# Performance work log

Hardware: AMD Instinct MI355X
Metric: run time of the kernel (lower is better)

## Reference

```python
import jax, jax.numpy as jnp
import numpy as np

K = 3  # kernel size along the folded height sub-dimension

def setup_inputs() -> dict:
    key = jax.random.key(0)
    k1, k2 = jax.random.split(key)
    x = jax.random.normal(k1, (1, 48, 56, 56), dtype=jnp.float32)
    W = jax.random.normal(k2, (192, 48, 3), dtype=jnp.float32)
    return {"x": x, "W": W}

def reference(x, W):
    # x: (1,48,56,56) -> (1,48,8,7,56): split H=56 into (8,7)
    t = x.reshape(1, 48, 8, 7, 56)
    # unfold((3,1), padding=(1,0)) acting on the size-7 axis:
    # pad by 1 on each side, then gather K=3 shifted views.
    tp = jnp.pad(t, ((0, 0), (0, 0), (0, 0), (1, 1), (0, 0)))  # (1,48,8,9,56)
    # patches[l,j,n,k,o,m] = tp[l,j,n,o+k,m], o in [0,7), k in [0,3)
    patches = jnp.stack([tp[:, :, :, k:k + 7, :] for k in range(K)], axis=3)  # (1,48,8,3,7,56)
    # einsum 'ljnkom, ijk -> linom' with W (192,48,3)
    out = jnp.einsum('ljnkom,ijk->linom', patches, W)  # (1,192,8,7,56)
    return out.reshape(1, 192, 56, 56)
```

## Files before the change

kernel.cpp:

```cpp
#include <hip/hip_runtime.h>


#define CH_IN 48
#define CH_OUT 192
#define HW 56
#define SP 3136
#define NB 8
#define OB 7
#define M4 14
#define COLS (NB * M4)
#define NCOL (CH_OUT * COLS)
#define SEGS 4
#define JSEG (CH_IN / SEGS)

__device__ __forceinline__ void fma4(float4& a, float s, const float4& b) {
    a.x += s * b.x; a.y += s * b.y; a.z += s * b.z; a.w += s * b.w;
}
__device__ __forceinline__ void add4(float4& a, const float4& b) {
    a.x += b.x; a.y += b.y; a.z += b.z; a.w += b.w;
}

__global__ __launch_bounds__(256) void conv_split_kernel(const float* __restrict__ x,
                                                         const float* __restrict__ W,
                                                         float* __restrict__ out) {
    __shared__ float4 lds[SEGS][OB][64];

    const int c   = threadIdx.x & 63;
    const int seg = threadIdx.x >> 6;
    const int col = blockIdx.x * 64 + c;

    const int i   = col / COLS;
    const int rem = col % COLS;
    const int n   = rem / M4;
    const int m4  = rem % M4;

    const float* xcol = x + seg * (JSEG * SP) + n * (OB * HW) + m4 * 4;
    const float* wrow = W + i * (CH_IN * 3) + seg * (JSEG * 3);

    float4 acc[OB];
#pragma unroll
    for (int o = 0; o < OB; ++o) acc[o] = make_float4(0.f, 0.f, 0.f, 0.f);

#pragma unroll 4
    for (int j = 0; j < JSEG; ++j) {
        const float w0 = wrow[j * 3 + 0];
        const float w1 = wrow[j * 3 + 1];
        const float w2 = wrow[j * 3 + 2];

        const float* xj = xcol + j * SP;
        float4 xv[OB];
#pragma unroll
        for (int o = 0; o < OB; ++o)
            xv[o] = *reinterpret_cast<const float4*>(xj + o * HW);

#pragma unroll
        for (int o = 0; o < OB; ++o) {
            if (o > 0)      fma4(acc[o], w0, xv[o - 1]);
            fma4(acc[o], w1, xv[o]);
            if (o < OB - 1) fma4(acc[o], w2, xv[o + 1]);
        }
    }

#pragma unroll
    for (int o = 0; o < OB; ++o) lds[seg][o][c] = acc[o];
    __syncthreads();

    for (int t = threadIdx.x; t < OB * 64; t += 256) {
        const int o  = t >> 6;
        const int cc = t & 63;
        float4 s = lds[0][o][cc];
        add4(s, lds[1][o][cc]);
        add4(s, lds[2][o][cc]);
        add4(s, lds[3][o][cc]);

        const int col2 = blockIdx.x * 64 + cc;
        const int i2   = col2 / COLS;
        const int rem2 = col2 % COLS;
        const int n2   = rem2 / M4;
        const int m42  = rem2 % M4;
        *reinterpret_cast<float4*>(out + i2 * SP + n2 * (OB * HW) + o * HW + m42 * 4) = s;
    }
}

extern "C" void kernel_launch(void* const* d_in, const int* in_sizes, int n_in,
                              void* d_out, int out_size, void* d_ws, size_t ws_size,
                              hipStream_t stream) {
    const float* x = (const float*)d_in[0];
    const float* W = (const float*)d_in[1];
    float* out = (float*)d_out;

    const int grid = NCOL / 64;
    conv_split_kernel<<<grid, 256, 0, stream>>>(x, W, out);
}
```

Measured before the change: 62.23 us.

## Split input channels into eight segments with smaller 16-column blocks

Raises the reduction split over input channels from 4 to 8 segments and shrinks each block to 16 output columns with 128 threads, giving 1344 blocks instead of 336. The j loop (now 6 iterations) is fully unrolled. The aim is more parallelism and occupancy across the GPU's compute units. In exchange each block does more LDS reduction work relative to compute, and global loads become narrower because each wavefront covers only 16 columns.

```diff
diff --git a/kernel.cpp b/kernel.cpp
--- a/kernel.cpp
+++ b/kernel.cpp
@@ -5,13 +5,13 @@
 #define CH_OUT 192
 #define HW 56
 #define SP 3136
-#define NB 8
 #define OB 7
 #define M4 14
-#define COLS (NB * M4)
+#define COLS 112
 #define NCOL (CH_OUT * COLS)
-#define SEGS 4
+#define SEGS 8
 #define JSEG (CH_IN / SEGS)
+#define BCOL 16
 
 __device__ __forceinline__ void fma4(float4& a, float s, const float4& b) {
     a.x += s * b.x; a.y += s * b.y; a.z += s * b.z; a.w += s * b.w;
@@ -20,14 +20,14 @@
     a.x += b.x; a.y += b.y; a.z += b.z; a.w += b.w;
 }
 
-__global__ __launch_bounds__(256) void conv_split_kernel(const float* __restrict__ x,
-                                                         const float* __restrict__ W,
-                                                         float* __restrict__ out) {
-    __shared__ float4 lds[SEGS][OB][64];
+__global__ __launch_bounds__(128) void conv_split8_kernel(const float* __restrict__ x,
+                                                          const float* __restrict__ W,
+                                                          float* __restrict__ out) {
+    __shared__ float4 lds[SEGS][OB][BCOL];
 
-    const int c   = threadIdx.x & 63;
-    const int seg = threadIdx.x >> 6;
-    const int col = blockIdx.x * 64 + c;
+    const int c   = threadIdx.x & (BCOL - 1);
+    const int seg = threadIdx.x / BCOL;
+    const int col = blockIdx.x * BCOL + c;
 
     const int i   = col / COLS;
     const int rem = col % COLS;
@@ -41,7 +41,7 @@
 #pragma unroll
     for (int o = 0; o < OB; ++o) acc[o] = make_float4(0.f, 0.f, 0.f, 0.f);
 
-#pragma unroll 4
+#pragma unroll
     for (int j = 0; j < JSEG; ++j) {
         const float w0 = wrow[j * 3 + 0];
         const float w1 = wrow[j * 3 + 1];
@@ -65,15 +65,15 @@
     for (int o = 0; o < OB; ++o) lds[seg][o][c] = acc[o];
     __syncthreads();
 
-    for (int t = threadIdx.x; t < OB * 64; t += 256) {
-        const int o  = t >> 6;
-        const int cc = t & 63;
+    const int t = threadIdx.x;
+    if (t < OB * BCOL) {
+        const int o  = t / BCOL;
+        const int cc = t & (BCOL - 1);
         float4 s = lds[0][o][cc];
-        add4(s, lds[1][o][cc]);
-        add4(s, lds[2][o][cc]);
-        add4(s, lds[3][o][cc]);
+#pragma unroll
+        for (int sgi = 1; sgi < SEGS; ++sgi) add4(s, lds[sgi][o][cc]);
 
-        const int col2 = blockIdx.x * 64 + cc;
+        const int col2 = blockIdx.x * BCOL + cc;
         const int i2   = col2 / COLS;
         const int rem2 = col2 % COLS;
         const int n2   = rem2 / M4;
@@ -89,6 +89,6 @@
     const float* W = (const float*)d_in[1];
     float* out = (float*)d_out;
 
-    const int grid = NCOL / 64;
-    conv_split_kernel<<<grid, 256, 0, stream>>>(x, W, out);
+    const int grid = NCOL / BCOL;
+    conv_split8_kernel<<<grid, 128, 0, stream>>>(x, W, out);
 }
```

Result: no change. 62.67 us (+0.7%).
